# Kernel optimization log

Measured on AMD Instinct MI355X. Metric: run time of the kernel, lower is better.

The kernel has to match this reference:

```python
import jax, jax.numpy as jnp
import numpy as np

B, T, C = 2, 2048, 1024
H, KV, HD = 16, 4, 64  # n_head, n_kv_head, head_dim = C // H


def apply_rotary_emb(x, cos, sin):
    d = x.shape[-1] // 2
    x1, x2 = x[..., :d], x[..., d:]
    return jnp.concatenate([x1 * cos + x2 * sin, -x1 * sin + x2 * cos], axis=-1)


def rms_norm(x):
    return x * jax.lax.rsqrt(jnp.mean(jnp.square(x), axis=-1, keepdims=True) + 1e-6)


def setup_inputs() -> dict:
    key = jax.random.key(0)
    ks = jax.random.split(key, 7)
    std = 0.02
    return {
        "x": jax.random.normal(ks[0], (B, T, C), jnp.float32),
        "cos": jax.random.normal(ks[1], (1, T, 1, HD // 2), jnp.float32),
        "sin": jax.random.normal(ks[2], (1, T, 1, HD // 2), jnp.float32),
        "Wq": jax.random.normal(ks[3], (C, H * HD), jnp.float32) * std,
        "Wk": jax.random.normal(ks[4], (C, KV * HD), jnp.float32) * std,
        "Wv": jax.random.normal(ks[5], (C, KV * HD), jnp.float32) * std,
        "Wo": jax.random.normal(ks[6], (C, C), jnp.float32) * std,
    }


def reference(x, cos, sin, Wq, Wk, Wv, Wo):
    b, t, c = x.shape
    q = (x @ Wq).reshape(b, t, H, HD)
    k = (x @ Wk).reshape(b, t, KV, HD)
    v = (x @ Wv).reshape(b, t, KV, HD)
    q = rms_norm(apply_rotary_emb(q, cos, sin))
    k = rms_norm(apply_rotary_emb(k, cos, sin))
    # GQA: repeat kv heads
    n_rep = H // KV
    k = jnp.repeat(k, n_rep, axis=2)
    v = jnp.repeat(v, n_rep, axis=2)
    # causal attention (flax dot_product_attention semantics)
    scale = 1.0 / jnp.sqrt(jnp.asarray(HD, x.dtype))
    logits = jnp.einsum('bqhd,bkhd->bhqk', q, k) * scale
    causal = jnp.tril(jnp.ones((t, t), bool))
    neg = jnp.finfo(x.dtype).min
    logits = jnp.where(causal[None, None], logits, neg)
    w = jax.nn.softmax(logits, axis=-1)
    y = jnp.einsum('bhqk,bkhd->bqhd', w, v).reshape(b, t, c)
    return y @ Wo
```

## Files before the change

kernel.cpp:

```cpp
#include <hip/hip_runtime.h>
#include <hip/hip_bf16.h>

#define B_   2
#define T_   2048
#define C_   1024
#define H_   16
#define KV_  4
#define HD_  64
#define M_   (B_*T_)
#define NQKV_ 1536
#define PST_ 72
#define M8L2E_ 11.5415603f

typedef __bf16 bf16x8 __attribute__((ext_vector_type(8)));
typedef float  f32x4  __attribute__((ext_vector_type(4)));

static __device__ __forceinline__ unsigned short f2bf(float f) {
    __hip_bfloat16 h = __float2bfloat16(f);
    return __builtin_bit_cast(unsigned short, h);
}
static __device__ __forceinline__ unsigned int pk2(float a, float b) {
    return (unsigned int)f2bf(a) | ((unsigned int)f2bf(b) << 16);
}

__global__ void prep_kernel(const float* __restrict__ x, unsigned short* __restrict__ xb,
                            const float* __restrict__ Wq, const float* __restrict__ Wk,
                            const float* __restrict__ Wv, const float* __restrict__ Wo,
                            unsigned short* __restrict__ wtqkv, unsigned short* __restrict__ wto) {
    __shared__ float tile[32][33];
    int bid = blockIdx.x;
    if (bid < 4096) {
        int i = (bid * 256 + threadIdx.x) * 4;
        float4 v = *(const float4*)(x + i);
        ushort4 o = make_ushort4(f2bf(v.x), f2bf(v.y), f2bf(v.z), f2bf(v.w));
        *(ushort4*)(xb + i) = o;
        return;
    }
    bid -= 4096;
    const float* src; unsigned short* dst; int s, nlog;
    if (bid < 1024)      { src = Wq; dst = wtqkv;               s = bid;        nlog = 5; }
    else if (bid < 1280) { src = Wk; dst = wtqkv + 1024 * 1024; s = bid - 1024; nlog = 3; }
    else if (bid < 1536) { src = Wv; dst = wtqkv + 1280 * 1024; s = bid - 1280; nlog = 3; }
    else                 { src = Wo; dst = wto;                 s = bid - 1536; nlog = 5; }
    int N  = 32 << nlog;
    int k0 = (s >> nlog) * 32, n0 = (s & ((1 << nlog) - 1)) * 32;
    int lr = threadIdx.x >> 5, lc = threadIdx.x & 31;
    #pragma unroll
    for (int i = 0; i < 4; i++) {
        int r = lr + i * 8;
        tile[r][lc] = src[(k0 + r) * N + n0 + lc];
    }
    __syncthreads();
    #pragma unroll
    for (int i = 0; i < 4; i++) {
        int r = lr + i * 8;
        dst[(n0 + r) * 1024 + k0 + lc] = f2bf(tile[lc][r]);
    }
}

template <typename T, bool ROPE>
__global__ __launch_bounds__(256) void gemm_kernel(const unsigned short* __restrict__ A,
                                                   const unsigned short* __restrict__ Bt,
                                                   T* __restrict__ Cm, int Ni,
                                                   const float* __restrict__ cosb,
                                                   const float* __restrict__ sinb,
                                                   unsigned short* __restrict__ vtb) {
    __shared__ __align__(16) unsigned short As[2][128 * 32];
    __shared__ __align__(16) unsigned short Bs[2][64 * 32];
    int head = blockIdx.x;
    int m0 = blockIdx.y * 128;
    int n0 = head * 64;
    int tid = threadIdx.x;
    int w = tid >> 6, lane = tid & 63;
    int col = lane & 15, quad = lane >> 4;
    int wm = w * 32;
    int ar = tid >> 2, ak = (tid & 3) * 8;

    f32x4 acc[2][4];
    #pragma unroll
    for (int mt = 0; mt < 2; mt++)
        #pragma unroll
        for (int nt = 0; nt < 4; nt++) acc[mt][nt] = (f32x4){0.f, 0.f, 0.f, 0.f};

    for (int k0 = 0; k0 < 1024; k0 += 64) {
        #pragma unroll
        for (int hh = 0; hh < 2; hh++) {
            __builtin_amdgcn_global_load_lds(
                (const __attribute__((address_space(1))) unsigned int*)(A + (size_t)(m0 + ar) * 1024 + k0 + hh * 32 + ak),
                (__attribute__((address_space(3))) unsigned int*)(&As[hh][ar * 32 + ak]), 16, 0, 0);
            __builtin_amdgcn_global_load_lds(
                (const __attribute__((address_space(1))) unsigned int*)(A + (size_t)(m0 + ar + 64) * 1024 + k0 + hh * 32 + ak),
                (__attribute__((address_space(3))) unsigned int*)(&As[hh][(ar + 64) * 32 + ak]), 16, 0, 0);
            __builtin_amdgcn_global_load_lds(
                (const __attribute__((address_space(1))) unsigned int*)(Bt + (size_t)(n0 + ar) * 1024 + k0 + hh * 32 + ak),
                (__attribute__((address_space(3))) unsigned int*)(&Bs[hh][ar * 32 + ak]), 16, 0, 0);
        }
        __syncthreads();
        bf16x8 af[2][2], bfr[4][2];
        #pragma unroll
        for (int hh = 0; hh < 2; hh++) {
            #pragma unroll
            for (int mt = 0; mt < 2; mt++) af[mt][hh]  = *(const bf16x8*)&As[hh][(wm + mt * 16 + col) * 32 + quad * 8];
            #pragma unroll
            for (int nt = 0; nt < 4; nt++) bfr[nt][hh] = *(const bf16x8*)&Bs[hh][(nt * 16 + col) * 32 + quad * 8];
        }
        #pragma unroll
        for (int hh = 0; hh < 2; hh++)
            #pragma unroll
            for (int mt = 0; mt < 2; mt++)
                #pragma unroll
                for (int nt = 0; nt < 4; nt++)
                    acc[mt][nt] = __builtin_amdgcn_mfma_f32_16x16x32_bf16(af[mt][hh], bfr[nt][hh], acc[mt][nt], 0, 0, 0);
        __syncthreads();
    }

    if constexpr (ROPE) {
        if (head >= H_ + KV_) {
            int kvh = head - (H_ + KV_);
            int b = m0 >> 11;
            #pragma unroll
            for (int mt = 0; mt < 2; mt++) {
                int tb = (m0 + wm + mt * 16 + quad * 4) & (T_ - 1);
                #pragma unroll
                for (int nt = 0; nt < 4; nt++) {
                    int d = nt * 16 + col;
                    uint2 pv;
                    pv.x = pk2(acc[mt][nt][0], acc[mt][nt][1]);
                    pv.y = pk2(acc[mt][nt][2], acc[mt][nt][3]);
                    *(uint2*)&vtb[((size_t)((b * KV_ + kvh) * 64 + d)) * T_ + tb] = pv;
                }
            }
            return;
        }
        #pragma unroll
        for (int mt = 0; mt < 2; mt++)
            #pragma unroll
            for (int r = 0; r < 4; r++) {
                int t = (m0 + wm + mt * 16 + quad * 4 + r) & (T_ - 1);
                float nv[4];
                #pragma unroll
                for (int nt = 0; nt < 4; nt++) {
                    int i = (nt & 1) * 16 + col;
                    float c = cosb[t * 32 + i], s = sinb[t * 32 + i];
                    float v = acc[mt][nt][r], p = acc[mt][nt ^ 2][r];
                    nv[nt] = (nt < 2) ? (v * c + p * s) : (v * c - p * s);
                }
                float sq = nv[0] * nv[0] + nv[1] * nv[1] + nv[2] * nv[2] + nv[3] * nv[3];
                sq += __shfl_xor(sq, 1, 64);
                sq += __shfl_xor(sq, 2, 64);
                sq += __shfl_xor(sq, 4, 64);
                sq += __shfl_xor(sq, 8, 64);
                float rr = rsqrtf(sq * (1.0f / 64.0f) + 1e-6f);
                if (head < H_) rr *= 0.125f * 1.44269504f;
                #pragma unroll
                for (int nt = 0; nt < 4; nt++) acc[mt][nt][r] = nv[nt] * rr;
            }
    }

    #pragma unroll
    for (int mt = 0; mt < 2; mt++)
        #pragma unroll
        for (int nt = 0; nt < 4; nt++)
            #pragma unroll
            for (int r = 0; r < 4; r++) {
                size_t idx = (size_t)(m0 + wm + mt * 16 + quad * 4 + r) * Ni + n0 + nt * 16 + col;
                if constexpr (sizeof(T) == 2) Cm[idx] = f2bf(acc[mt][nt][r]);
                else                          Cm[idx] = acc[mt][nt][r];
            }
}

__global__ __launch_bounds__(256) void attn_kernel(const unsigned short* __restrict__ qkvb,
                                                   const unsigned short* __restrict__ vtb,
                                                   unsigned short* __restrict__ yb) {
    __shared__ __align__(16) char smem[4 * 32 * 64 * 4];
    __shared__ float lbuf[4][32];

    int bh = blockIdx.x & 31;
    int pi = blockIdx.x >> 5;
    int b = bh >> 4, h = bh & 15, kvh = h >> 2;
    int tid = threadIdx.x;
    int w = tid >> 6, lane = tid & 63;
    int col = lane & 15, quad = lane >> 4;

    unsigned short* Ps = (unsigned short*)smem + w * (32 * PST_);
    float* Obuf = (float*)smem;

    const unsigned short* kptr = qkvb + (size_t)(b * T_) * NQKV_ + 1024 + kvh * 64;
    const unsigned short* vptr = vtb + (size_t)((b * KV_ + kvh) * 64) * T_;

    bf16x8 ones;
    #pragma unroll
    for (int j = 0; j < 8; j++) ones[j] = (__bf16)1.0f;

    for (int ti = 0; ti < 2; ti++) {
        int qt = ti ? pi : 63 - pi;
        int t0 = qt * 32;
        int nkt = (t0 + 95) >> 6;
        int we = ti ? 3 - w : w;

        bf16x8 aq[2][2];
        #pragma unroll
        for (int ntq = 0; ntq < 2; ntq++)
            #pragma unroll
            for (int step = 0; step < 2; step++)
                aq[ntq][step] = *(const bf16x8*)&qkvb[(size_t)(b * T_ + t0 + ntq * 16 + col) * NQKV_
                                                      + h * 64 + quad * 8 + step * 32];

        f32x4 o[2][4], lacc[2];
        #pragma unroll
        for (int mt = 0; mt < 2; mt++) {
            lacc[mt] = (f32x4){0.f, 0.f, 0.f, 0.f};
            #pragma unroll
            for (int nt = 0; nt < 4; nt++) o[mt][nt] = (f32x4){0.f, 0.f, 0.f, 0.f};
        }

        for (int kt = we; kt < nkt; kt += 4) {
            f32x4 sacc[4][2];
            #pragma unroll
            for (int mtk = 0; mtk < 4; mtk++)
                #pragma unroll
                for (int ntq = 0; ntq < 2; ntq++) sacc[mtk][ntq] = (f32x4){0.f, 0.f, 0.f, 0.f};
            #pragma unroll
            for (int step = 0; step < 2; step++) {
                bf16x8 kb[4];
                #pragma unroll
                for (int mtk = 0; mtk < 4; mtk++)
                    kb[mtk] = *(const bf16x8*)&kptr[(size_t)(kt * 64 + mtk * 16 + col) * NQKV_
                                                    + quad * 8 + step * 32];
                #pragma unroll
                for (int mtk = 0; mtk < 4; mtk++)
                    #pragma unroll
                    for (int ntq = 0; ntq < 2; ntq++)
                        sacc[mtk][ntq] = __builtin_amdgcn_mfma_f32_16x16x32_bf16(kb[mtk], aq[ntq][step], sacc[mtk][ntq], 0, 0, 0);
            }
            bf16x8 vb[2][4];
            #pragma unroll
            for (int step = 0; step < 2; step++)
                #pragma unroll
                for (int ntd = 0; ntd < 4; ntd++)
                    vb[step][ntd] = *(const bf16x8*)&vptr[(size_t)(ntd * 16 + col) * T_
                                                          + kt * 64 + quad * 8 + step * 32];
            if (kt == nkt - 1) {
                #pragma unroll
                for (int mtk = 0; mtk < 4; mtk++)
                    #pragma unroll
                    for (int ntq = 0; ntq < 2; ntq++)
                        #pragma unroll
                        for (int r = 0; r < 4; r++)
                            if (kt * 64 + mtk * 16 + quad * 4 + r > t0 + ntq * 16 + col)
                                sacc[mtk][ntq][r] = -1e30f;
            }
            #pragma unroll
            for (int mtk = 0; mtk < 4; mtk++)
                #pragma unroll
                for (int ntq = 0; ntq < 2; ntq++) {
                    uint2 pw;
                    pw.x = pk2(__builtin_amdgcn_exp2f(sacc[mtk][ntq][0] - M8L2E_),
                               __builtin_amdgcn_exp2f(sacc[mtk][ntq][1] - M8L2E_));
                    pw.y = pk2(__builtin_amdgcn_exp2f(sacc[mtk][ntq][2] - M8L2E_),
                               __builtin_amdgcn_exp2f(sacc[mtk][ntq][3] - M8L2E_));
                    *(uint2*)&Ps[(ntq * 16 + col) * PST_ + mtk * 16 + quad * 4] = pw;
                }
            #pragma unroll
            for (int step = 0; step < 2; step++) {
                bf16x8 ap[2];
                #pragma unroll
                for (int mtq = 0; mtq < 2; mtq++)
                    ap[mtq] = *(const bf16x8*)&Ps[(mtq * 16 + col) * PST_ + quad * 8 + step * 32];
                #pragma unroll
                for (int ntd = 0; ntd < 4; ntd++)
                    #pragma unroll
                    for (int mtq = 0; mtq < 2; mtq++)
                        o[mtq][ntd] = __builtin_amdgcn_mfma_f32_16x16x32_bf16(ap[mtq], vb[step][ntd], o[mtq][ntd], 0, 0, 0);
                #pragma unroll
                for (int mtq = 0; mtq < 2; mtq++)
                    lacc[mtq] = __builtin_amdgcn_mfma_f32_16x16x32_bf16(ap[mtq], ones, lacc[mtq], 0, 0, 0);
            }
        }

        __syncthreads();
        #pragma unroll
        for (int mt = 0; mt < 2; mt++)
            #pragma unroll
            for (int nt = 0; nt < 4; nt++)
                #pragma unroll
                for (int r = 0; r < 4; r++)
                    Obuf[w * 2048 + (mt * 16 + quad * 4 + r) * 64 + nt * 16 + col] = o[mt][nt][r];
        if (col == 0) {
            #pragma unroll
            for (int mt = 0; mt < 2; mt++)
                #pragma unroll
                for (int r = 0; r < 4; r++)
                    lbuf[w][mt * 16 + quad * 4 + r] = lacc[mt][r];
        }
        __syncthreads();
        {
            int row = tid >> 3, d0 = (tid & 7) * 8;
            float ls = lbuf[0][row] + lbuf[1][row] + lbuf[2][row] + lbuf[3][row];
            float inv = 1.0f / ls;
            float s[8];
            #pragma unroll
            for (int j = 0; j < 8; j++) s[j] = 0.f;
            #pragma unroll
            for (int wv = 0; wv < 4; wv++) {
                f32x4 p0 = *(const f32x4*)&Obuf[wv * 2048 + row * 64 + d0];
                f32x4 p1 = *(const f32x4*)&Obuf[wv * 2048 + row * 64 + d0 + 4];
                #pragma unroll
                for (int j = 0; j < 4; j++) { s[j] += p0[j]; s[4 + j] += p1[j]; }
            }
            unsigned short o8[8];
            #pragma unroll
            for (int j = 0; j < 8; j++) o8[j] = f2bf(s[j] * inv);
            *(uint4*)&yb[(size_t)(b * T_ + t0 + row) * C_ + h * 64 + d0] = *(uint4*)o8;
        }
        __syncthreads();
    }
}

extern "C" void kernel_launch(void* const* d_in, const int* in_sizes, int n_in,
                              void* d_out, int out_size, void* d_ws, size_t ws_size,
                              hipStream_t stream) {
    const float* x    = (const float*)d_in[0];
    const float* cosb = (const float*)d_in[1];
    const float* sinb = (const float*)d_in[2];
    const float* Wq   = (const float*)d_in[3];
    const float* Wk   = (const float*)d_in[4];
    const float* Wv   = (const float*)d_in[5];
    const float* Wo   = (const float*)d_in[6];
    float* out = (float*)d_out;

    char* ws = (char*)d_ws;
    unsigned short* xb    = (unsigned short*)(ws);
    unsigned short* yb    = (unsigned short*)(ws);
    unsigned short* wtqkv = (unsigned short*)(ws + ( 8u << 20));
    unsigned short* wto   = (unsigned short*)(ws + (11u << 20));
    unsigned short* qkvb  = (unsigned short*)(ws + (13u << 20));
    unsigned short* vtb   = (unsigned short*)(ws + (25u << 20));

    prep_kernel<<<4096 + 2560, 256, 0, stream>>>(x, xb, Wq, Wk, Wv, Wo, wtqkv, wto);
    gemm_kernel<unsigned short, true><<<dim3(24, 32), 256, 0, stream>>>(xb, wtqkv, qkvb, NQKV_, cosb, sinb, vtb);
    attn_kernel<<<1024, 256, 0, stream>>>(qkvb, vtb, yb);
    gemm_kernel<float, false><<<dim3(16, 32), 256, 0, stream>>>(yb, wto, out, C_, nullptr, nullptr, nullptr);
}
```

Before: 192.2 us.

## Keep softmax probabilities in registers instead of LDS round-trip for PV MFMA

The P tile is no longer written to LDS and read back. The exp results are packed into bf16 pairs and fed straight into the PV MFMA A operand, using a permuted k-ordering that matches the S accumulator layout. V is loaded in matching 4-element chunks so both operands use the same permuted k index. This removes LDS stores, loads and their latency from the inner loop, along with the __syncthreads that guarded reuse of the shared P/O buffer. The cost is more register pressure and narrower 8-byte V loads.

```diff
diff --git a/kernel.cpp b/kernel.cpp
--- a/kernel.cpp
+++ b/kernel.cpp
@@ -9,7 +9,6 @@
 #define HD_  64
 #define M_   (B_*T_)
 #define NQKV_ 1536
-#define PST_ 72
 #define M8L2E_ 11.5415603f
 
 typedef __bf16 bf16x8 __attribute__((ext_vector_type(8)));
@@ -21,6 +20,10 @@
 }
 static __device__ __forceinline__ unsigned int pk2(float a, float b) {
     return (unsigned int)f2bf(a) | ((unsigned int)f2bf(b) << 16);
+}
+static __device__ __forceinline__ bf16x8 cat8(uint2 a, uint2 b) {
+    uint4 u; u.x = a.x; u.y = a.y; u.z = b.x; u.w = b.y;
+    return __builtin_bit_cast(bf16x8, u);
 }
 
 __global__ void prep_kernel(const float* __restrict__ x, unsigned short* __restrict__ xb,
@@ -172,7 +175,7 @@
 __global__ __launch_bounds__(256) void attn_kernel(const unsigned short* __restrict__ qkvb,
                                                    const unsigned short* __restrict__ vtb,
                                                    unsigned short* __restrict__ yb) {
-    __shared__ __align__(16) char smem[4 * 32 * 64 * 4];
+    __shared__ __align__(16) float Obuf[4 * 32 * 64];
     __shared__ float lbuf[4][32];
 
     int bh = blockIdx.x & 31;
@@ -182,9 +185,6 @@
     int w = tid >> 6, lane = tid & 63;
     int col = lane & 15, quad = lane >> 4;
 
-    unsigned short* Ps = (unsigned short*)smem + w * (32 * PST_);
-    float* Obuf = (float*)smem;
-
     const unsigned short* kptr = qkvb + (size_t)(b * T_) * NQKV_ + 1024 + kvh * 64;
     const unsigned short* vptr = vtb + (size_t)((b * KV_ + kvh) * 64) * T_;
 
@@ -215,6 +215,13 @@
         }
 
         for (int kt = we; kt < nkt; kt += 4) {
+            uint2 vraw[4][4];
+            #pragma unroll
+            for (int mtk = 0; mtk < 4; mtk++)
+                #pragma unroll
+                for (int ntd = 0; ntd < 4; ntd++)
+                    vraw[mtk][ntd] = *(const uint2*)&vptr[(size_t)(ntd * 16 + col) * T_
+                                                          + kt * 64 + mtk * 16 + quad * 4];
             f32x4 sacc[4][2];
             #pragma unroll
             for (int mtk = 0; mtk < 4; mtk++)
@@ -233,52 +240,42 @@
                     for (int ntq = 0; ntq < 2; ntq++)
                         sacc[mtk][ntq] = __builtin_amdgcn_mfma_f32_16x16x32_bf16(kb[mtk], aq[ntq][step], sacc[mtk][ntq], 0, 0, 0);
             }
-            bf16x8 vb[2][4];
-            #pragma unroll
-            for (int step = 0; step < 2; step++)
-                #pragma unroll
-                for (int ntd = 0; ntd < 4; ntd++)
-                    vb[step][ntd] = *(const bf16x8*)&vptr[(size_t)(ntd * 16 + col) * T_
-                                                          + kt * 64 + quad * 8 + step * 32];
-            if (kt == nkt - 1) {
-                #pragma unroll
-                for (int mtk = 0; mtk < 4; mtk++)
-                    #pragma unroll
-                    for (int ntq = 0; ntq < 2; ntq++)
+            bool diag = (kt == nkt - 1);
+            uint2 pw[4][2];
+            #pragma unroll
+            for (int mtk = 0; mtk < 4; mtk++)
+                #pragma unroll
+                for (int ntq = 0; ntq < 2; ntq++) {
+                    if (diag) {
                         #pragma unroll
                         for (int r = 0; r < 4; r++)
                             if (kt * 64 + mtk * 16 + quad * 4 + r > t0 + ntq * 16 + col)
                                 sacc[mtk][ntq][r] = -1e30f;
-            }
-            #pragma unroll
-            for (int mtk = 0; mtk < 4; mtk++)
-                #pragma unroll
-                for (int ntq = 0; ntq < 2; ntq++) {
-                    uint2 pw;
-                    pw.x = pk2(__builtin_amdgcn_exp2f(sacc[mtk][ntq][0] - M8L2E_),
-                               __builtin_amdgcn_exp2f(sacc[mtk][ntq][1] - M8L2E_));
-                    pw.y = pk2(__builtin_amdgcn_exp2f(sacc[mtk][ntq][2] - M8L2E_),
-                               __builtin_amdgcn_exp2f(sacc[mtk][ntq][3] - M8L2E_));
-                    *(uint2*)&Ps[(ntq * 16 + col) * PST_ + mtk * 16 + quad * 4] = pw;
+                    }
+                    pw[mtk][ntq].x = pk2(__builtin_amdgcn_exp2f(sacc[mtk][ntq][0] - M8L2E_),
+                                         __builtin_amdgcn_exp2f(sacc[mtk][ntq][1] - M8L2E_));
+                    pw[mtk][ntq].y = pk2(__builtin_amdgcn_exp2f(sacc[mtk][ntq][2] - M8L2E_),
+                                         __builtin_amdgcn_exp2f(sacc[mtk][ntq][3] - M8L2E_));
                 }
             #pragma unroll
-            for (int step = 0; step < 2; step++) {
+            for (int pr = 0; pr < 2; pr++) {
+                int ma = pr * 2, mb = pr * 2 + 1;
                 bf16x8 ap[2];
                 #pragma unroll
-                for (int mtq = 0; mtq < 2; mtq++)
-                    ap[mtq] = *(const bf16x8*)&Ps[(mtq * 16 + col) * PST_ + quad * 8 + step * 32];
-                #pragma unroll
-                for (int ntd = 0; ntd < 4; ntd++)
+                for (int ntq = 0; ntq < 2; ntq++) ap[ntq] = cat8(pw[ma][ntq], pw[mb][ntq]);
+                #pragma unroll
+                for (int ntd = 0; ntd < 4; ntd++) {
+                    bf16x8 vb = cat8(vraw[ma][ntd], vraw[mb][ntd]);
                     #pragma unroll
-                    for (int mtq = 0; mtq < 2; mtq++)
-                        o[mtq][ntd] = __builtin_amdgcn_mfma_f32_16x16x32_bf16(ap[mtq], vb[step][ntd], o[mtq][ntd], 0, 0, 0);
-                #pragma unroll
-                for (int mtq = 0; mtq < 2; mtq++)
-                    lacc[mtq] = __builtin_amdgcn_mfma_f32_16x16x32_bf16(ap[mtq], ones, lacc[mtq], 0, 0, 0);
-            }
-        }
-
-        __syncthreads();
+                    for (int ntq = 0; ntq < 2; ntq++)
+                        o[ntq][ntd] = __builtin_amdgcn_mfma_f32_16x16x32_bf16(ap[ntq], vb, o[ntq][ntd], 0, 0, 0);
+                }
+                #pragma unroll
+                for (int ntq = 0; ntq < 2; ntq++)
+                    lacc[ntq] = __builtin_amdgcn_mfma_f32_16x16x32_bf16(ap[ntq], ones, lacc[ntq], 0, 0, 0);
+            }
+        }
+
         #pragma unroll
         for (int mt = 0; mt < 2; mt++)
             #pragma unroll
```

Result: slower. 218.1 us (+13.5%).

## Store K and V in MFMA-fragment tiled layouts for contiguous attention loads

Applied to the files above, without the earlier changes.

The QKV GEMM epilogue now writes K and V into separate buffers laid out in 16x32 / 32-wide fragment tiles that match the attention kernel's MFMA operand order. Q keeps its own row stride of 1024. The attention kernel then reads each K and V fragment from a contiguous 1 KB block instead of strided rows of the wide QKV matrix. This aims at better coalescing and cache-line use in the attention inner loop. The cost is scattered 2-byte stores for K in the GEMM epilogue.

```diff
diff --git a/kernel.cpp b/kernel.cpp
--- a/kernel.cpp
+++ b/kernel.cpp
@@ -8,7 +8,7 @@
 #define KV_  4
 #define HD_  64
 #define M_   (B_*T_)
-#define NQKV_ 1536
+#define QSTR_ 1024
 #define PST_ 72
 #define M8L2E_ 11.5415603f
 
@@ -64,7 +64,8 @@
                                                    T* __restrict__ Cm, int Ni,
                                                    const float* __restrict__ cosb,
                                                    const float* __restrict__ sinb,
-                                                   unsigned short* __restrict__ vtb) {
+                                                   unsigned short* __restrict__ vfb,
+                                                   unsigned short* __restrict__ ktb) {
     __shared__ __align__(16) unsigned short As[2][128 * 32];
     __shared__ __align__(16) unsigned short Bs[2][64 * 32];
     int head = blockIdx.x;
@@ -115,19 +116,19 @@
     }
 
     if constexpr (ROPE) {
+        int b = m0 >> 11;
         if (head >= H_ + KV_) {
             int kvh = head - (H_ + KV_);
-            int b = m0 >> 11;
+            unsigned short* vbase = vfb + (size_t)(b * KV_ + kvh) * (T_ * 64);
             #pragma unroll
             for (int mt = 0; mt < 2; mt++) {
                 int tb = (m0 + wm + mt * 16 + quad * 4) & (T_ - 1);
                 #pragma unroll
                 for (int nt = 0; nt < 4; nt++) {
-                    int d = nt * 16 + col;
                     uint2 pv;
                     pv.x = pk2(acc[mt][nt][0], acc[mt][nt][1]);
                     pv.y = pk2(acc[mt][nt][2], acc[mt][nt][3]);
-                    *(uint2*)&vtb[((size_t)((b * KV_ + kvh) * 64 + d)) * T_ + tb] = pv;
+                    *(uint2*)&vbase[((tb >> 5) * 4 + nt) * 512 + col * 32 + (tb & 31)] = pv;
                 }
             }
             return;
@@ -155,6 +156,22 @@
                 #pragma unroll
                 for (int nt = 0; nt < 4; nt++) acc[mt][nt][r] = nv[nt] * rr;
             }
+        if (head >= H_) {
+            int kvh = head - H_;
+            unsigned short* kbase = ktb + (size_t)(b * KV_ + kvh) * (T_ * 64);
+            #pragma unroll
+            for (int mt = 0; mt < 2; mt++)
+                #pragma unroll
+                for (int r = 0; r < 4; r++) {
+                    int t = (m0 + wm + mt * 16 + quad * 4 + r) & (T_ - 1);
+                    #pragma unroll
+                    for (int nt = 0; nt < 4; nt++) {
+                        int dd = nt * 16 + col;
+                        kbase[(t >> 4) * 1024 + (dd >> 5) * 512 + (t & 15) * 32 + (dd & 31)] = f2bf(acc[mt][nt][r]);
+                    }
+                }
+            return;
+        }
     }
 
     #pragma unroll
@@ -170,7 +187,8 @@
 }
 
 __global__ __launch_bounds__(256) void attn_kernel(const unsigned short* __restrict__ qkvb,
-                                                   const unsigned short* __restrict__ vtb,
+                                                   const unsigned short* __restrict__ ktb,
+                                                   const unsigned short* __restrict__ vfb,
                                                    unsigned short* __restrict__ yb) {
     __shared__ __align__(16) char smem[4 * 32 * 64 * 4];
     __shared__ float lbuf[4][32];
@@ -185,8 +203,8 @@
     unsigned short* Ps = (unsigned short*)smem + w * (32 * PST_);
     float* Obuf = (float*)smem;
 
-    const unsigned short* kptr = qkvb + (size_t)(b * T_) * NQKV_ + 1024 + kvh * 64;
-    const unsigned short* vptr = vtb + (size_t)((b * KV_ + kvh) * 64) * T_;
+    const unsigned short* kfb = ktb + (size_t)(b * KV_ + kvh) * (T_ * 64);
+    const unsigned short* vfp = vfb + (size_t)(b * KV_ + kvh) * (T_ * 64);
 
     bf16x8 ones;
     #pragma unroll
@@ -203,7 +221,7 @@
         for (int ntq = 0; ntq < 2; ntq++)
             #pragma unroll
             for (int step = 0; step < 2; step++)
-                aq[ntq][step] = *(const bf16x8*)&qkvb[(size_t)(b * T_ + t0 + ntq * 16 + col) * NQKV_
+                aq[ntq][step] = *(const bf16x8*)&qkvb[(size_t)(b * T_ + t0 + ntq * 16 + col) * QSTR_
                                                       + h * 64 + quad * 8 + step * 32];
 
         f32x4 o[2][4], lacc[2];
@@ -225,8 +243,7 @@
                 bf16x8 kb[4];
                 #pragma unroll
                 for (int mtk = 0; mtk < 4; mtk++)
-                    kb[mtk] = *(const bf16x8*)&kptr[(size_t)(kt * 64 + mtk * 16 + col) * NQKV_
-                                                    + quad * 8 + step * 32];
+                    kb[mtk] = *(const bf16x8*)&kfb[(kt * 4 + mtk) * 1024 + step * 512 + col * 32 + quad * 8];
                 #pragma unroll
                 for (int mtk = 0; mtk < 4; mtk++)
                     #pragma unroll
@@ -238,8 +255,7 @@
             for (int step = 0; step < 2; step++)
                 #pragma unroll
                 for (int ntd = 0; ntd < 4; ntd++)
-                    vb[step][ntd] = *(const bf16x8*)&vptr[(size_t)(ntd * 16 + col) * T_
-                                                          + kt * 64 + quad * 8 + step * 32];
+                    vb[step][ntd] = *(const bf16x8*)&vfp[((kt * 2 + step) * 4 + ntd) * 512 + col * 32 + quad * 8];
             if (kt == nkt - 1) {
                 #pragma unroll
                 for (int mtk = 0; mtk < 4; mtk++)
@@ -335,10 +351,11 @@
     unsigned short* wtqkv = (unsigned short*)(ws + ( 8u << 20));
     unsigned short* wto   = (unsigned short*)(ws + (11u << 20));
     unsigned short* qkvb  = (unsigned short*)(ws + (13u << 20));
-    unsigned short* vtb   = (unsigned short*)(ws + (25u << 20));
+    unsigned short* vfb   = (unsigned short*)(ws + (21u << 20));
+    unsigned short* ktb   = (unsigned short*)(ws + (23u << 20));
 
     prep_kernel<<<4096 + 2560, 256, 0, stream>>>(x, xb, Wq, Wk, Wv, Wo, wtqkv, wto);
-    gemm_kernel<unsigned short, true><<<dim3(24, 32), 256, 0, stream>>>(xb, wtqkv, qkvb, NQKV_, cosb, sinb, vtb);
-    attn_kernel<<<1024, 256, 0, stream>>>(qkvb, vtb, yb);
-    gemm_kernel<float, false><<<dim3(16, 32), 256, 0, stream>>>(yb, wto, out, C_, nullptr, nullptr, nullptr);
-}
+    gemm_kernel<unsigned short, true><<<dim3(24, 32), 256, 0, stream>>>(xb, wtqkv, qkvb, QSTR_, cosb, sinb, vfb, ktb);
+    attn_kernel<<<1024, 256, 0, stream>>>(qkvb, ktb, vfb, yb);
+    gemm_kernel<float, false><<<dim3(16, 32), 256, 0, stream>>>(yb, wto, out, C_, nullptr, nullptr, nullptr, nullptr);
+}
```

Result: faster. 167.0 us (-13.1%).
